# Optimization experiments

Hardware: AMD Instinct MI355X
Metric: run time of the kernel (lower is better)

The kernel has to match this reference:

```python
import jax, jax.numpy as jnp
import numpy as np

B = 262144  # batch of configurations
J = 24      # revolute joints in a serial chain (base -> link_1 -> ... -> link_J)


def setup_inputs() -> dict:
    key = jax.random.key(0)
    k1, k2, k3, k4 = jax.random.split(key, 4)
    joint_angles = jax.random.normal(k1, (B, J), dtype=jnp.float32)
    xyz = jax.random.uniform(k2, (J, 3), dtype=jnp.float32) * 0.2          # joint origin translation
    rpy = jax.random.uniform(k3, (J, 3), dtype=jnp.float32) * 0.5          # joint origin fixed euler
    axis = jax.random.uniform(k4, (J, 3), dtype=jnp.float32) + 0.1        # revolute axis (unnormalized, as in URDF)
    return {"joint_angles": joint_angles, "xyz": xyz, "rpy": rpy, "axis": axis}


def _euler_to_rot(rpy):
    # (J,3) -> (J,3,3), Rz(y) @ Ry(p) @ Rx(r)
    r, p, y = rpy[:, 0], rpy[:, 1], rpy[:, 2]
    cr, sr = jnp.cos(r), jnp.sin(r)
    cp, sp = jnp.cos(p), jnp.sin(p)
    cy, sy = jnp.cos(y), jnp.sin(y)
    row0 = jnp.stack([cy * cp, cy * sp * sr - sy * cr, cy * sp * cr + sy * sr], -1)
    row1 = jnp.stack([sy * cp, sy * sp * sr + cy * cr, sy * sp * cr - cy * sr], -1)
    row2 = jnp.stack([-sp, cp * sr, cp * cr], -1)
    return jnp.stack([row0, row1, row2], -2)


def _rodrigues(aa):
    # (B,3) axis-angle -> (B,3,3). R = ca*I + (1-ca)*kk^T + sa*[k]_x
    angle = jnp.linalg.norm(aa, axis=-1)
    k = aa / jnp.maximum(angle, 1e-6)[:, None]
    ca, sa = jnp.cos(angle), jnp.sin(angle)
    oc = 1.0 - ca
    kx, ky, kz = k[:, 0], k[:, 1], k[:, 2]
    row0 = jnp.stack([ca + kx * kx * oc, kx * ky * oc - kz * sa, kx * kz * oc + ky * sa], -1)
    row1 = jnp.stack([ky * kx * oc + kz * sa, ca + ky * ky * oc, ky * kz * oc - kx * sa], -1)
    row2 = jnp.stack([kz * kx * oc - ky * sa, kz * ky * oc + kx * sa, ca + kz * kz * oc], -1)
    R = jnp.stack([row0, row1, row2], -2)
    eye = jnp.eye(3, dtype=aa.dtype)
    return jnp.where((angle == 0.0)[:, None, None], eye, R)


def reference(joint_angles, xyz, rpy, axis):
    bs, nj = joint_angles.shape
    dt = joint_angles.dtype
    # fixed per-joint origin transforms (J,4,4)
    Ro = _euler_to_rot(rpy)
    T_origin = (jnp.zeros((nj, 4, 4), dt)
                .at[:, :3, :3].set(Ro)
                .at[:, :3, 3].set(xyz)
                .at[:, 3, 3].set(1.0))

    def step(T_parent, per_joint):
        To, ax, theta = per_joint  # (4,4), (3,), (B,)
        R = _rodrigues(ax[None, :] * theta[:, None])          # (B,3,3)
        T_joint = (jnp.zeros((bs, 4, 4), dt)
                   .at[:, :3, :3].set(R)
                   .at[:, 3, 3].set(1.0))
        T_mid = jnp.einsum('ij,bjk->bik', To, T_joint)        # T_origin @ T_joint
        T_child = jnp.einsum('bij,bjk->bik', T_parent, T_mid) # chain product
        return T_child, T_child[:, :3, 3]

    T_base = jnp.broadcast_to(jnp.eye(4, dtype=dt), (bs, 4, 4))
    _, pos = jax.lax.scan(step, T_base, (T_origin, axis, joint_angles.T))  # pos: (J,B,3)
    # base link position (identity transform) comes first, as in link_names order
    pos = jnp.concatenate([jnp.zeros((1, bs, 3), dt), pos], axis=0)        # (J+1,B,3)
    return jnp.transpose(pos, (1, 0, 2)).reshape(bs, -1)                   # (B, 3*(J+1))
```

## Files before the change

### kernel.cpp

```cpp
#include <hip/hip_runtime.h>

#define NJ 24
#define BLK 128
#define OUTW 75
#define ROWF (BLK * OUTW)
#define CW 12

__global__ __launch_bounds__(BLK, 4) void fk_main_kernel(
    const float* __restrict__ ang,
    const float* __restrict__ xyz,
    const float* __restrict__ rpy,
    const float* __restrict__ axis,
    float* __restrict__ out)
{
    __shared__ float lcst[NJ * CW];
    __shared__ float4 buf4[ROWF / 4];
    float* buf = (float*)buf4;

    const int tid = threadIdx.x;
    const long long b0 = (long long)blockIdx.x * BLK;

    const float4* gA4 = (const float4*)(ang + (b0 + tid) * NJ);
    float4 a0 = gA4[0], a1 = gA4[1], a2 = gA4[2], a3 = gA4[3], a4 = gA4[4], a5 = gA4[5];
    float th[NJ] = {a0.x,a0.y,a0.z,a0.w, a1.x,a1.y,a1.z,a1.w,
                    a2.x,a2.y,a2.z,a2.w, a3.x,a3.y,a3.z,a3.w,
                    a4.x,a4.y,a4.z,a4.w, a5.x,a5.y,a5.z,a5.w};

    if (tid < NJ) {
        const int j = tid;
        float r = rpy[j*3+0] * 0.5f, p = rpy[j*3+1] * 0.5f, yv = rpy[j*3+2] * 0.5f;
        float sr, cr, sp, cp, sy, cy;
        __sincosf(r, &sr, &cr);
        __sincosf(p, &sp, &cp);
        __sincosf(yv, &sy, &cy);
        float qw = cr*cp*cy + sr*sp*sy;
        float qx = sr*cp*cy - cr*sp*sy;
        float qy = cr*sp*cy + sr*cp*sy;
        float qz = cr*cp*sy - sr*sp*cy;
        float ax = axis[j*3+0], ay = axis[j*3+1], az = axis[j*3+2];
        float n = sqrtf(ax*ax + ay*ay + az*az);
        float inv = 1.0f / fmaxf(n, 1e-6f);
        float ux = ax*inv, uy = ay*inv, uz = az*inv;
        float* c = &lcst[j * CW];
        c[0] = qw; c[1] = qx; c[2] = qy; c[3] = qz;
        c[4] = -(qx*ux + qy*uy + qz*uz);
        c[5] = qw*ux + qy*uz - qz*uy;
        c[6] = qw*uy + qz*ux - qx*uz;
        c[7] = qw*uz + qx*uy - qy*ux;
        c[8] = xyz[j*3+0]; c[9] = xyz[j*3+1]; c[10] = xyz[j*3+2];
        c[11] = n * 0.5f;
    }
    __syncthreads();

    float Qw = 1.f, Qx = 0.f, Qy = 0.f, Qz = 0.f;
    float t0 = 0.f, t1 = 0.f, t2 = 0.f;
    float* ob = &buf[tid * OUTW];
    ob[0] = 0.f; ob[1] = 0.f; ob[2] = 0.f;

    #pragma unroll
    for (int j = 0; j < NJ; ++j) {
        const float* c = &lcst[j * CW];
        float h = th[j] * c[11];
        float s, cq;
        __sincosf(h, &s, &cq);
        float lw = cq*c[0] + s*c[4];
        float lx = cq*c[1] + s*c[5];
        float ly = cq*c[2] + s*c[6];
        float lz = cq*c[3] + s*c[7];
        float vx = c[8], vy = c[9], vz = c[10];
        float px = Qy*vz - Qz*vy + Qw*vx;
        float py = Qz*vx - Qx*vz + Qw*vy;
        float pz = Qx*vy - Qy*vx + Qw*vz;
        t0 += vx + 2.0f*(Qy*pz - Qz*py);
        t1 += vy + 2.0f*(Qz*px - Qx*pz);
        t2 += vz + 2.0f*(Qx*py - Qy*px);
        float nw = Qw*lw - Qx*lx - Qy*ly - Qz*lz;
        float nx = Qw*lx + Qx*lw + Qy*lz - Qz*ly;
        float ny = Qw*ly - Qx*lz + Qy*lw + Qz*lx;
        float nz = Qw*lz + Qx*ly - Qy*lx + Qz*lw;
        Qw = nw; Qx = nx; Qy = ny; Qz = nz;

        ob[3*(j+1)+0] = t0;
        ob[3*(j+1)+1] = t1;
        ob[3*(j+1)+2] = t2;
    }
    __syncthreads();

    float4* gO = (float4*)(out + b0 * OUTW);
    #pragma unroll
    for (int k = 0; k < (ROWF/4 + BLK - 1) / BLK; ++k) {
        int i = tid + k * BLK;
        if (i < ROWF / 4) gO[i] = buf4[i];
    }
}

extern "C" void kernel_launch(void* const* d_in, const int* in_sizes, int n_in,
                              void* d_out, int out_size, void* d_ws, size_t ws_size,
                              hipStream_t stream) {
    const float* ang  = (const float*)d_in[0];
    const float* xyz  = (const float*)d_in[1];
    const float* rpy  = (const float*)d_in[2];
    const float* axis = (const float*)d_in[3];
    float* out = (float*)d_out;

    const int B = in_sizes[0] / NJ;
    const int grid = (B + BLK - 1) / BLK;
    fk_main_kernel<<<grid, BLK, 0, stream>>>(ang, xyz, rpy, axis, out);
}
```

Measured before the change: 30.21 us.

## Process two chunks per block with per-wave LDS staging and prefetch next angles

Each block now handles two consecutive 128-row chunks. Every wave stages its own 64 rows in LDS and writes them to global memory with only a wave-level LDS wait, so the block-wide barrier before the store is gone. The next chunk's angles are loaded before the current chunk's store so the load latency overlaps the writeback. This halves the grid, amortizes the per-block constant setup, and lowers the occupancy hint from 4 to 2. The grid size now assumes B is divisible by 256, and correctness of the per-wave LDS reuse depends on wave-local ordering.

New measurement: 28.58 us. 1.06x faster.

```diff
diff --git a/kernel.cpp b/kernel.cpp
--- a/kernel.cpp
+++ b/kernel.cpp
@@ -3,10 +3,12 @@
 #define NJ 24
 #define BLK 128
 #define OUTW 75
-#define ROWF (BLK * OUTW)
+#define WROWS 64
+#define WBUF (WROWS * OUTW)
+#define CPB 2
 #define CW 12
 
-__global__ __launch_bounds__(BLK, 4) void fk_main_kernel(
+__global__ __launch_bounds__(BLK, 2) void fk_main_kernel(
     const float* __restrict__ ang,
     const float* __restrict__ xyz,
     const float* __restrict__ rpy,
@@ -14,17 +16,16 @@
     float* __restrict__ out)
 {
     __shared__ float lcst[NJ * CW];
-    __shared__ float4 buf4[ROWF / 4];
-    float* buf = (float*)buf4;
+    __shared__ float buf[(BLK / 64) * WBUF];
 
     const int tid = threadIdx.x;
-    const long long b0 = (long long)blockIdx.x * BLK;
+    const int wv = tid >> 6, ln = tid & 63;
+    float* wbuf = &buf[wv * WBUF];
 
-    const float4* gA4 = (const float4*)(ang + (b0 + tid) * NJ);
-    float4 a0 = gA4[0], a1 = gA4[1], a2 = gA4[2], a3 = gA4[3], a4 = gA4[4], a5 = gA4[5];
-    float th[NJ] = {a0.x,a0.y,a0.z,a0.w, a1.x,a1.y,a1.z,a1.w,
-                    a2.x,a2.y,a2.z,a2.w, a3.x,a3.y,a3.z,a3.w,
-                    a4.x,a4.y,a4.z,a4.w, a5.x,a5.y,a5.z,a5.w};
+    const long long chunk0 = (long long)blockIdx.x * CPB;
+
+    const float4* gA = (const float4*)(ang + (chunk0 * BLK + tid) * NJ);
+    float4 A0 = gA[0], A1 = gA[1], A2 = gA[2], A3 = gA[3], A4 = gA[4], A5 = gA[5];
 
     if (tid < NJ) {
         const int j = tid;
@@ -52,45 +53,64 @@
     }
     __syncthreads();
 
-    float Qw = 1.f, Qx = 0.f, Qy = 0.f, Qz = 0.f;
-    float t0 = 0.f, t1 = 0.f, t2 = 0.f;
-    float* ob = &buf[tid * OUTW];
-    ob[0] = 0.f; ob[1] = 0.f; ob[2] = 0.f;
+    #pragma unroll
+    for (int c = 0; c < CPB; ++c) {
+        float th[NJ] = {A0.x,A0.y,A0.z,A0.w, A1.x,A1.y,A1.z,A1.w,
+                        A2.x,A2.y,A2.z,A2.w, A3.x,A3.y,A3.z,A3.w,
+                        A4.x,A4.y,A4.z,A4.w, A5.x,A5.y,A5.z,A5.w};
 
-    #pragma unroll
-    for (int j = 0; j < NJ; ++j) {
-        const float* c = &lcst[j * CW];
-        float h = th[j] * c[11];
-        float s, cq;
-        __sincosf(h, &s, &cq);
-        float lw = cq*c[0] + s*c[4];
-        float lx = cq*c[1] + s*c[5];
-        float ly = cq*c[2] + s*c[6];
-        float lz = cq*c[3] + s*c[7];
-        float vx = c[8], vy = c[9], vz = c[10];
-        float px = Qy*vz - Qz*vy + Qw*vx;
-        float py = Qz*vx - Qx*vz + Qw*vy;
-        float pz = Qx*vy - Qy*vx + Qw*vz;
-        t0 += vx + 2.0f*(Qy*pz - Qz*py);
-        t1 += vy + 2.0f*(Qz*px - Qx*pz);
-        t2 += vz + 2.0f*(Qx*py - Qy*px);
-        float nw = Qw*lw - Qx*lx - Qy*ly - Qz*lz;
-        float nx = Qw*lx + Qx*lw + Qy*lz - Qz*ly;
-        float ny = Qw*ly - Qx*lz + Qy*lw + Qz*lx;
-        float nz = Qw*lz + Qx*ly - Qy*lx + Qz*lw;
-        Qw = nw; Qx = nx; Qy = ny; Qz = nz;
+        if (c) {
+            asm volatile("s_waitcnt lgkmcnt(0)" ::: "memory");
+            __builtin_amdgcn_sched_barrier(0);
+        }
 
-        ob[3*(j+1)+0] = t0;
-        ob[3*(j+1)+1] = t1;
-        ob[3*(j+1)+2] = t2;
-    }
-    __syncthreads();
+        float Qw = 1.f, Qx = 0.f, Qy = 0.f, Qz = 0.f;
+        float t0 = 0.f, t1 = 0.f, t2 = 0.f;
+        float* ob = wbuf + ln * OUTW;
+        ob[0] = 0.f; ob[1] = 0.f; ob[2] = 0.f;
 
-    float4* gO = (float4*)(out + b0 * OUTW);
-    #pragma unroll
-    for (int k = 0; k < (ROWF/4 + BLK - 1) / BLK; ++k) {
-        int i = tid + k * BLK;
-        if (i < ROWF / 4) gO[i] = buf4[i];
+        #pragma unroll
+        for (int j = 0; j < NJ; ++j) {
+            const float* cc = &lcst[j * CW];
+            float h = th[j] * cc[11];
+            float s, cq;
+            __sincosf(h, &s, &cq);
+            float lw = cq*cc[0] + s*cc[4];
+            float lx = cq*cc[1] + s*cc[5];
+            float ly = cq*cc[2] + s*cc[6];
+            float lz = cq*cc[3] + s*cc[7];
+            float vx = cc[8], vy = cc[9], vz = cc[10];
+            float px = Qy*vz - Qz*vy + Qw*vx;
+            float py = Qz*vx - Qx*vz + Qw*vy;
+            float pz = Qx*vy - Qy*vx + Qw*vz;
+            t0 += vx + 2.0f*(Qy*pz - Qz*py);
+            t1 += vy + 2.0f*(Qz*px - Qx*pz);
+            t2 += vz + 2.0f*(Qx*py - Qy*px);
+            float nw = Qw*lw - Qx*lx - Qy*ly - Qz*lz;
+            float nx = Qw*lx + Qx*lw + Qy*lz - Qz*ly;
+            float ny = Qw*ly - Qx*lz + Qy*lw + Qz*lx;
+            float nz = Qw*lz + Qx*ly - Qy*lx + Qz*lw;
+            Qw = nw; Qx = nx; Qy = ny; Qz = nz;
+            ob[3*(j+1)+0] = t0;
+            ob[3*(j+1)+1] = t1;
+            ob[3*(j+1)+2] = t2;
+        }
+
+        if (c + 1 < CPB) {
+            const float4* gN = (const float4*)(ang + ((chunk0 + c + 1) * BLK + tid) * NJ);
+            A0 = gN[0]; A1 = gN[1]; A2 = gN[2]; A3 = gN[3]; A4 = gN[4]; A5 = gN[5];
+        }
+
+        asm volatile("s_waitcnt lgkmcnt(0)" ::: "memory");
+        __builtin_amdgcn_sched_barrier(0);
+
+        float4* gO = (float4*)(out + (chunk0 + c) * (BLK * OUTW)) + wv * (WBUF / 4);
+        const float4* lb = (const float4*)wbuf;
+        #pragma unroll
+        for (int k = 0; k < 19; ++k) {
+            int i = k * 64 + ln;
+            if (i < WBUF / 4) gO[i] = lb[i];
+        }
     }
 }
 
@@ -104,6 +124,6 @@
     float* out = (float*)d_out;
 
     const int B = in_sizes[0] / NJ;
-    const int grid = (B + BLK - 1) / BLK;
+    const int grid = B / (BLK * CPB);
     fk_main_kernel<<<grid, BLK, 0, stream>>>(ang, xyz, rpy, axis, out);
 }
```

## Broadcast joint constants via readlane and write output rows directly from registers

Applied to the files above, without the earlier changes.

Each wavefront now computes the per-joint constants in its own lanes and broadcasts them with readlane, so the shared-memory constant table and both block barriers go away. Each thread keeps its 75 output floats in registers and writes its row straight to global memory with unaligned 4-wide, 2-wide and scalar stores, replacing the shared-memory staging buffer and the coalesced copy-out. This frees LDS and removes the syncs, but every lane now strides 300 bytes apart, so the output stores are much less coalesced and register pressure goes up. The grid also drops its rounding up and assumes B is a multiple of the block size.

Result: slower. 41.76 us (+38.2%).

```diff
diff --git a/kernel.cpp b/kernel.cpp
--- a/kernel.cpp
+++ b/kernel.cpp
@@ -1,10 +1,15 @@
 #include <hip/hip_runtime.h>
+
+typedef float f4 __attribute__((ext_vector_type(4)));
+typedef f4 __attribute__((aligned(4))) f4u;
+typedef float f2 __attribute__((ext_vector_type(2)));
+typedef f2 __attribute__((aligned(4))) f2u;
 
 #define NJ 24
 #define BLK 128
 #define OUTW 75
-#define ROWF (BLK * OUTW)
-#define CW 12
+
+#define RL(v, j) __int_as_float(__builtin_amdgcn_readlane(__float_as_int(v), (j)))
 
 __global__ __launch_bounds__(BLK, 4) void fk_main_kernel(
     const float* __restrict__ ang,
@@ -13,21 +18,18 @@
     const float* __restrict__ axis,
     float* __restrict__ out)
 {
-    __shared__ float lcst[NJ * CW];
-    __shared__ float4 buf4[ROWF / 4];
-    float* buf = (float*)buf4;
+    const int tid = threadIdx.x;
+    const int ln  = tid & 63;
 
-    const int tid = threadIdx.x;
-    const long long b0 = (long long)blockIdx.x * BLK;
+    const long long row = (long long)blockIdx.x * BLK + tid;
+    const f4* gA = (const f4*)(ang + row * NJ);
+    f4 A[6];
+    #pragma unroll
+    for (int k = 0; k < 6; ++k) A[k] = gA[k];
 
-    const float4* gA4 = (const float4*)(ang + (b0 + tid) * NJ);
-    float4 a0 = gA4[0], a1 = gA4[1], a2 = gA4[2], a3 = gA4[3], a4 = gA4[4], a5 = gA4[5];
-    float th[NJ] = {a0.x,a0.y,a0.z,a0.w, a1.x,a1.y,a1.z,a1.w,
-                    a2.x,a2.y,a2.z,a2.w, a3.x,a3.y,a3.z,a3.w,
-                    a4.x,a4.y,a4.z,a4.w, a5.x,a5.y,a5.z,a5.w};
-
-    if (tid < NJ) {
-        const int j = tid;
+    float c0=0,c1=0,c2=0,c3=0,c4=0,c5=0,c6=0,c7=0,c8=0,c9=0,c10=0,c11=0;
+    if (ln < NJ) {
+        const int j = ln;
         float r = rpy[j*3+0] * 0.5f, p = rpy[j*3+1] * 0.5f, yv = rpy[j*3+2] * 0.5f;
         float sr, cr, sp, cp, sy, cy;
         __sincosf(r, &sr, &cr);
@@ -41,33 +43,34 @@
         float n = sqrtf(ax*ax + ay*ay + az*az);
         float inv = 1.0f / fmaxf(n, 1e-6f);
         float ux = ax*inv, uy = ay*inv, uz = az*inv;
-        float* c = &lcst[j * CW];
-        c[0] = qw; c[1] = qx; c[2] = qy; c[3] = qz;
-        c[4] = -(qx*ux + qy*uy + qz*uz);
-        c[5] = qw*ux + qy*uz - qz*uy;
-        c[6] = qw*uy + qz*ux - qx*uz;
-        c[7] = qw*uz + qx*uy - qy*ux;
-        c[8] = xyz[j*3+0]; c[9] = xyz[j*3+1]; c[10] = xyz[j*3+2];
-        c[11] = n * 0.5f;
+        c0 = qw; c1 = qx; c2 = qy; c3 = qz;
+        c4 = -(qx*ux + qy*uy + qz*uz);
+        c5 = qw*ux + qy*uz - qz*uy;
+        c6 = qw*uy + qz*ux - qx*uz;
+        c7 = qw*uz + qx*uy - qy*ux;
+        c8 = xyz[j*3+0]; c9 = xyz[j*3+1]; c10 = xyz[j*3+2];
+        c11 = n * 0.5f;
     }
-    __syncthreads();
 
+    float o[OUTW];
+    o[0] = 0.f; o[1] = 0.f; o[2] = 0.f;
     float Qw = 1.f, Qx = 0.f, Qy = 0.f, Qz = 0.f;
     float t0 = 0.f, t1 = 0.f, t2 = 0.f;
-    float* ob = &buf[tid * OUTW];
-    ob[0] = 0.f; ob[1] = 0.f; ob[2] = 0.f;
 
     #pragma unroll
     for (int j = 0; j < NJ; ++j) {
-        const float* c = &lcst[j * CW];
-        float h = th[j] * c[11];
+        float qa0 = RL(c0, j), qa1 = RL(c1, j), qa2 = RL(c2, j), qa3 = RL(c3, j);
+        float qb0 = RL(c4, j), qb1 = RL(c5, j), qb2 = RL(c6, j), qb3 = RL(c7, j);
+        float vx  = RL(c8, j), vy  = RL(c9, j), vz  = RL(c10, j);
+        float hn  = RL(c11, j);
+
+        float h = A[j >> 2][j & 3] * hn;
         float s, cq;
         __sincosf(h, &s, &cq);
-        float lw = cq*c[0] + s*c[4];
-        float lx = cq*c[1] + s*c[5];
-        float ly = cq*c[2] + s*c[6];
-        float lz = cq*c[3] + s*c[7];
-        float vx = c[8], vy = c[9], vz = c[10];
+        float lw = cq*qa0 + s*qb0;
+        float lx = cq*qa1 + s*qb1;
+        float ly = cq*qa2 + s*qb2;
+        float lz = cq*qa3 + s*qb3;
         float px = Qy*vz - Qz*vy + Qw*vx;
         float py = Qz*vx - Qx*vz + Qw*vy;
         float pz = Qx*vy - Qy*vx + Qw*vz;
@@ -79,19 +82,19 @@
         float ny = Qw*ly - Qx*lz + Qy*lw + Qz*lx;
         float nz = Qw*lz + Qx*ly - Qy*lx + Qz*lw;
         Qw = nw; Qx = nx; Qy = ny; Qz = nz;
+        o[3*(j+1)+0] = t0;
+        o[3*(j+1)+1] = t1;
+        o[3*(j+1)+2] = t2;
+    }
 
-        ob[3*(j+1)+0] = t0;
-        ob[3*(j+1)+1] = t1;
-        ob[3*(j+1)+2] = t2;
+    float* gR = out + row * OUTW;
+    #pragma unroll
+    for (int k = 0; k < 18; ++k) {
+        f4 v = { o[4*k+0], o[4*k+1], o[4*k+2], o[4*k+3] };
+        *(f4u*)(gR + 4*k) = v;
     }
-    __syncthreads();
-
-    float4* gO = (float4*)(out + b0 * OUTW);
-    #pragma unroll
-    for (int k = 0; k < (ROWF/4 + BLK - 1) / BLK; ++k) {
-        int i = tid + k * BLK;
-        if (i < ROWF / 4) gO[i] = buf4[i];
-    }
+    { f2 v = { o[72], o[73] }; *(f2u*)(gR + 72) = v; }
+    gR[74] = o[74];
 }
 
 extern "C" void kernel_launch(void* const* d_in, const int* in_sizes, int n_in,
@@ -104,6 +107,6 @@
     float* out = (float*)d_out;
 
     const int B = in_sizes[0] / NJ;
-    const int grid = (B + BLK - 1) / BLK;
+    const int grid = B / BLK;
     fk_main_kernel<<<grid, BLK, 0, stream>>>(ang, xyz, rpy, axis, out);
 }
```
